# Kernel optimization log

Hardware: AMD Instinct MI355X
Metric: run time of the kernel (lower is better)

The kernel has to match this reference:

```python
import jax, jax.numpy as jnp
import numpy as np

B = 512      # batch
T = 16       # tokens per instruction
V = 1000     # vocab
E = 4        # num_experts
K = 1        # active experts per layer
NLAYERS = 3
TOPK_LOGIC = 32


def _conv(x, w, b, stride=2):
    # x: [B,Cin,H,W], w: [Cout,Cin,3,3] (OIHW), padding=1, stride=2
    y = jax.lax.conv_general_dilated(
        x, w, window_strides=(stride, stride), padding=((1, 1), (1, 1)),
        dimension_numbers=('NCHW', 'OIHW', 'NCHW'))
    return y + b[None, :, None, None]


def _gated_conv(x, w, b, gate):
    # w: [E,Cout,Cin,3,3], b: [E,Cout], gate: [B,E] 0/1 mask
    # Faithful to original: all experts computed densely, then masked.
    outs = jax.vmap(lambda wi, bi: _conv(x, wi, bi))(w, b)  # [E,B,Cout,H',W']
    return jnp.einsum('ebchw,be->bchw', outs, gate)


def _topk_mask(logits, k):
    # 0/1 mask with ones at the top-k positions along the last axis
    _, idx = jax.lax.top_k(logits, k)
    return jnp.sum(jax.nn.one_hot(idx, logits.shape[-1], dtype=logits.dtype), axis=-2)


def setup_inputs() -> dict:
    key = jax.random.key(0)
    ks = jax.random.split(key, 16)
    def rn(k, shape, s=0.05):
        return jax.random.normal(k, shape, jnp.float32) * s
    return dict(
        img=jax.random.normal(ks[0], (B, 12, 56, 56), jnp.float32),
        text=jax.random.randint(ks[1], (B, T), 0, V),
        prev_action=jax.random.randint(ks[2], (B,), 0, 7),
        emb_table=rn(ks[3], (V, 32), 1.0),
        r_w1=rn(ks[4], (32, 64)), r_b1=jnp.zeros((64,), jnp.float32),
        r_w2=rn(ks[5], (64, NLAYERS * E)), r_b2=jnp.zeros((NLAYERS * E,), jnp.float32),
        l_w1=rn(ks[6], (32, 64)), l_b1=jnp.zeros((64,), jnp.float32),
        l_w2=rn(ks[7], (64, 256)), l_b2=jnp.zeros((256,), jnp.float32),
        c1_w=rn(ks[8], (E, 32, 12, 3, 3)), c1_b=jnp.zeros((E, 32), jnp.float32),
        c2_w=rn(ks[9], (E, 64, 32, 3, 3)), c2_b=jnp.zeros((E, 64), jnp.float32),
        c3_w=rn(ks[10], (E, 128, 64, 3, 3)), c3_b=jnp.zeros((E, 128), jnp.float32),
        act_emb=rn(ks[11], (7, 16), 1.0),
        f_w=rn(ks[12], (6272 + 32 + 16, 256)), f_b=jnp.zeros((256,), jnp.float32),
        h_w=rn(ks[13], (256, 5)), h_b=jnp.zeros((5,), jnp.float32),
    )


def reference(img, text, prev_action, emb_table, r_w1, r_b1, r_w2, r_b2,
              l_w1, l_b1, l_w2, l_b2, c1_w, c1_b, c2_w, c2_b, c3_w, c3_b,
              act_emb, f_w, f_b, h_w, h_b):
    # EmbeddingBag(mode='mean') over token dim
    lang = jnp.mean(emb_table[text], axis=1)                      # [B,32]
    # Router: MLP -> [B,3,E] logits, top-k scatter -> 0/1 mask
    rlog = (jax.nn.relu(lang @ r_w1 + r_b1) @ r_w2 + r_b2).reshape(-1, NLAYERS, E)
    masks = _topk_mask(rlog, K)                                   # [B,3,E]
    x = jax.nn.relu(_gated_conv(img, c1_w, c1_b, masks[:, 0, :])) # [B,32,28,28]
    x = jax.nn.relu(_gated_conv(x, c2_w, c2_b, masks[:, 1, :]))   # [B,64,14,14]
    x = jax.nn.relu(_gated_conv(x, c3_w, c3_b, masks[:, 2, :]))   # [B,128,7,7]
    vis = x.reshape(x.shape[0], -1)                               # [B,6272]
    act = act_emb[prev_action]                                    # [B,16]
    fused = jnp.concatenate([vis, lang, act], axis=1)             # [B,6320]
    hidden = fused @ f_w + f_b                                    # [B,256]
    logic = jax.nn.relu(lang @ l_w1 + l_b1) @ l_w2 + l_b2         # [B,256]
    lmask = _topk_mask(logic, TOPK_LOGIC)                         # [B,256]
    out = jax.nn.relu(hidden * lmask)                             # dropout is identity in eval
    logits = out @ h_w + h_b                                      # [B,5]
    return logits, rlog
```

## Files before the change

### kernel.cpp

```cpp
#include <hip/hip_runtime.h>
#include <hip/hip_bf16.h>


typedef __bf16 bf16x8 __attribute__((ext_vector_type(8)));
typedef float f32x4 __attribute__((ext_vector_type(4)));

__device__ __forceinline__ unsigned short f2bf(float f) {
  union { float f; unsigned u; } v; v.f = f;
  unsigned r = v.u + 0x7FFFu + ((v.u >> 16) & 1u);
  return (unsigned short)(r >> 16);
}

__device__ __forceinline__ int wswz(int b) { return b ^ (((b >> 7) & 3) << 4); }

__global__ __launch_bounds__(256) void prep_kernel(
    const int* __restrict__ text, const float* __restrict__ emb,
    const float* __restrict__ r_w1, const float* __restrict__ r_b1,
    const float* __restrict__ r_w2, const float* __restrict__ r_b2,
    const float* __restrict__ l_w1, const float* __restrict__ l_b1,
    const float* __restrict__ l_w2, const float* __restrict__ l_b2,
    const float* __restrict__ act_emb, const int* __restrict__ pa,
    const float* __restrict__ c1_w, const float* __restrict__ c2_w,
    const float* __restrict__ c3_w, const float* __restrict__ fw,
    float* __restrict__ rlog_out, int* __restrict__ eidx, float* __restrict__ lmask,
    unsigned short* __restrict__ tailb,
    unsigned short* __restrict__ wb1, unsigned short* __restrict__ wb2,
    unsigned short* __restrict__ wb3, unsigned short* __restrict__ fwT) {
  __shared__ __align__(16) char shm[64 * 72 * 2];
  const int blk = blockIdx.x;
  const int tid = threadIdx.x;

  if (blk < 512) {
    int b = blk;
    int t = tid;
    __shared__ float lg[32];
    __shared__ float hr[64];
    __shared__ float hl[64];
    __shared__ float rl[12];
    __shared__ float lgc[256];

    if (t < 32) {
      const int* tb = text + b * 16;
      float s = 0.f;
#pragma unroll
      for (int tok = 0; tok < 16; ++tok) s += emb[tb[tok] * 32 + t];
      lg[t] = s * 0.0625f;
    }
    __syncthreads();

    if (t < 64) {
      float s1 = r_b1[t], s2 = l_b1[t];
      for (int k = 0; k < 32; ++k) {
        float lv = lg[k];
        s1 += lv * r_w1[k * 64 + t];
        s2 += lv * l_w1[k * 64 + t];
      }
      hr[t] = fmaxf(s1, 0.f);
      hl[t] = fmaxf(s2, 0.f);
    }
    if (t < 64) {
      float v = 0.f;
      if (t < 32) v = lg[t];
      else if (t < 48) v = act_emb[pa[b] * 16 + (t - 32)];
      tailb[b * 64 + t] = f2bf(v);
    }
    __syncthreads();

    if (t < 12) {
      float s = r_b2[t];
      for (int k = 0; k < 64; ++k) s += hr[k] * r_w2[k * 12 + t];
      rl[t] = s;
      rlog_out[b * 12 + t] = s;
    }
    {
      float s = l_b2[t];
      for (int k = 0; k < 64; ++k) s += hl[k] * l_w2[k * 256 + t];
      lgc[t] = s;
    }
    __syncthreads();

    if (t < 3) {
      int best = 0;
      float bv = rl[t * 4];
      for (int e = 1; e < 4; ++e) {
        float v = rl[t * 4 + e];
        if (v > bv) { bv = v; best = e; }
      }
      eidx[b * 3 + t] = best;
    }
    {
      float v = lgc[t];
      int cnt = 0;
      for (int k = 0; k < 256; ++k) {
        float u = lgc[k];
        cnt += (u > v) || (u == v && k < t);
      }
      lmask[b * 256 + t] = (cnt < 32) ? 1.f : 0.f;
    }
  } else if (blk < 2080) {
    int idx = (blk - 512) * 256 + tid;
    if (idx < 24576) {
      int k = idx % 192, ec = idx / 192;
      float v = 0.f;
      if (k < 144) {
        int g = k >> 4, ci = k & 15;
        if (ci < 12) v = c1_w[ec * 108 + ci * 9 + g];
      }
      wb1[idx] = f2bf(v);
    } else if (idx < 106496) {
      int i2 = idx - 24576;
      int k = i2 % 320, ec = i2 / 320;
      float v = 0.f;
      if (k < 288) {
        int g = k >> 5, ci = k & 31;
        v = c2_w[ec * 288 + ci * 9 + g];
      }
      wb2[i2] = f2bf(v);
    } else {
      int i3 = idx - 106496;
      int k = i3 % 576, ec = i3 / 576;
      int g = k >> 6, ci = k & 63;
      wb3[i3] = f2bf(c3_w[ec * 576 + ci * 9 + g]);
    }
  } else {
    unsigned short(*tl)[72] = (unsigned short(*)[72])shm;
    int fb = blk - 2080;
    int kblk = fb >> 2, nblk = fb & 3;
    int n0 = nblk * 64;
    int k0 = kblk * 64;
    int rl = tid >> 2;
    int c4 = (tid & 3) * 16;
    int srow;
    bool valid;
    if (kblk < 98) {
      int p = kblk >> 1;
      int c0 = (kblk & 1) * 64;
      srow = (c0 + rl) * 49 + p;
      valid = true;
    } else {
      srow = 6272 + rl;
      valid = (rl < 48);
    }
#pragma unroll
    for (int h = 0; h < 4; ++h) {
      float4 v = valid ? *(const float4*)&fw[(size_t)srow * 256 + n0 + c4 + h * 4]
                       : (float4){0.f, 0.f, 0.f, 0.f};
      tl[rl][c4 + h * 4 + 0] = f2bf(v.x);
      tl[rl][c4 + h * 4 + 1] = f2bf(v.y);
      tl[rl][c4 + h * 4 + 2] = f2bf(v.z);
      tl[rl][c4 + h * 4 + 3] = f2bf(v.w);
    }
    __syncthreads();
    int nloc = tid >> 2;
    int kc = (tid & 3) * 16;
    unsigned short vv[16];
#pragma unroll
    for (int i = 0; i < 16; ++i) vv[i] = tl[kc + i][nloc];
    unsigned short* dst = fwT + (size_t)(n0 + nloc) * 6336 + k0 + kc;
    *(uint4*)dst = *(const uint4*)&vv[0];
    *(uint4*)(dst + 8) = *(const uint4*)&vv[8];
  }
}

__global__ __launch_bounds__(256) void bucket_kernel(const int* __restrict__ eidx,
                                                     int* __restrict__ cnt,
                                                     int* __restrict__ perm) {
  int l = blockIdx.x;
  __shared__ int el[512];
  __shared__ int cc[4];
  int t = threadIdx.x;
  el[t] = eidx[t * 3 + l];
  el[t + 256] = eidx[(t + 256) * 3 + l];
  __syncthreads();
  if (t < 4) {
    int c = 0;
    for (int b = 0; b < 512; ++b) c += (el[b] == t);
    cc[t] = c;
    cnt[l * 4 + t] = c;
  }
  __syncthreads();
#pragma unroll
  for (int rep = 0; rep < 2; ++rep) {
    int b = t + rep * 256;
    int e = el[b];
    int rank = 0;
    for (int bp = 0; bp < b; ++bp) rank += (el[bp] == e);
    int off = 0;
    for (int ee = 0; ee < e; ++ee) off += cc[ee];
    perm[l * 512 + off + rank] = b;
  }
}

__global__ __launch_bounds__(256) void conv1_fused(
    const float* __restrict__ img, const unsigned short* __restrict__ wb,
    const float* __restrict__ bias, const int* __restrict__ eidx,
    unsigned short* __restrict__ out) {
  const int s = blockIdx.x / 7;
  const int t = blockIdx.x % 7;
  const int e = eidx[s * 3];
  __shared__ __align__(16) char win[25536];
  __shared__ __align__(16) char ldsB[3 * 4096];
  const int tid = threadIdx.x;
  const int lane = tid & 63;
  const int wid = tid >> 6;
  const int wm0 = wid * 32;

  const int p0 = t * 128;
  const int ohmin = p0 / 28;
  const int ih0 = ohmin * 2 - 1;

  {
    uint4 z; z.x = z.y = z.z = z.w = 0u;
    for (int i = tid; i < 1596; i += 256) ((uint4*)win)[i] = z;
  }
  {
    const unsigned short* wbe = wb + e * (32 * 192);
#pragma unroll
    for (int c = 0; c < 3; ++c) {
      int cc = tid + 256 * c;
      int n = cc / 24, cb = cc - n * 24;
      int kt = cb >> 3, cbl = cb & 7;
      uint4 v = *(const uint4*)(wbe + n * 192 + cb * 8);
      *(uint4*)(ldsB + kt * 4096 + n * 128 + ((cbl * 16) ^ ((n & 7) << 4))) = v;
    }
  }
  __syncthreads();

  for (int task = tid; task < 312; task += 256) {
    int row = task >> 1, half = task & 1;
    int ci = row / 13, ihl = row - ci * 13;
    int ih = ih0 + ihl;
    if ((unsigned)ih < 56u) {
      const float* src = img + (size_t)s * 37632 + ci * 3136 + ih * 56 + half * 28;
      int base = (ihl * 57 + half * 28 + 1) * 32 + ci * 2;
#pragma unroll
      for (int u = 0; u < 7; ++u) {
        float4 v = *(const float4*)(src + u * 4);
        unsigned short w4[4] = {f2bf(v.x), f2bf(v.y), f2bf(v.z), f2bf(v.w)};
#pragma unroll
        for (int q = 0; q < 4; ++q) {
          int bp = base + (u * 4 + q) * 32;
          *(unsigned short*)(win + wswz(bp)) = w4[q];
        }
      }
    }
  }

  int ohl[2], owr[2];
#pragma unroll
  for (int mf = 0; mf < 2; ++mf) {
    int m = wm0 + mf * 16 + (lane & 15);
    int p = p0 + m;
    if (p > 783) p = 783;
    int oh = p / 28;
    owr[mf] = p - oh * 28;
    ohl[mf] = (oh - ohmin) * 2;
  }
  const int lg = lane >> 4;
  const int ci0 = (lg & 1) * 8;
  const int lgh = lg >> 1;
  int brdo[2], brx[2];
#pragma unroll
  for (int nf = 0; nf < 2; ++nf) {
    int n = nf * 16 + (lane & 15);
    brdo[nf] = n * 128;
    brx[nf] = (n & 7) << 4;
  }

  f32x4 acc[2][2];
#pragma unroll
  for (int mf = 0; mf < 2; ++mf)
#pragma unroll
    for (int nf = 0; nf < 2; ++nf) acc[mf][nf] = (f32x4){0.f, 0.f, 0.f, 0.f};

  __syncthreads();

#pragma unroll
  for (int kt = 0; kt < 3; ++kt) {
#pragma unroll
    for (int ks = 0; ks < 2; ++ks) {
      const int g = kt * 4 + ks * 2 + lgh;
      const int kh = g / 3;
      const int kw = g - kh * 3;
      const bool gv = (g < 9);
      bf16x8 af[2];
#pragma unroll
      for (int mf = 0; mf < 2; ++mf) {
        int iwp = owr[mf] * 2 + kw;
        int ihl = ohl[mf] + kh;
        int bp = gv ? ((ihl * 57 + iwp) * 32 + ci0 * 2)
                    : (13 * 57 * 32 + ci0 * 2);
        af[mf] = __builtin_bit_cast(bf16x8, *(const uint4*)(win + wswz(bp)));
      }
      bf16x8 bfv[2];
      const int cb = ks * 64 + ((lane >> 4) << 4);
#pragma unroll
      for (int nf = 0; nf < 2; ++nf)
        bfv[nf] = __builtin_bit_cast(bf16x8,
            *(const uint4*)(ldsB + kt * 4096 + brdo[nf] + (cb ^ brx[nf])));
#pragma unroll
      for (int mf = 0; mf < 2; ++mf)
#pragma unroll
        for (int nf = 0; nf < 2; ++nf)
          acc[mf][nf] = __builtin_amdgcn_mfma_f32_16x16x32_bf16(af[mf], bfv[nf], acc[mf][nf], 0, 0, 0);
    }
  }

  const int col = lane & 15;
  const int rg = (lane >> 4) * 4;
  const float b0 = bias[e * 32 + col];
  const float b1 = bias[e * 32 + 16 + col];
#pragma unroll
  for (int mf = 0; mf < 2; ++mf)
#pragma unroll
    for (int r = 0; r < 4; ++r) {
      int m = wm0 + mf * 16 + rg + r;
      int p = p0 + m;
      if (p < 784) {
        size_t ob = ((size_t)s * 784 + p) * 32;
        out[ob + col]      = f2bf(fmaxf(acc[mf][0][r] + b0, 0.f));
        out[ob + 16 + col] = f2bf(fmaxf(acc[mf][1][r] + b1, 0.f));
      }
    }
}

template<int CIN, int H, int OH, int KREAL, int KP, int COUT,
         int WGM, int WGN, int MF, int NF>
__global__ __launch_bounds__(256) void conv_mfma(
    const unsigned short* __restrict__ in, const unsigned short* __restrict__ wb,
    const float* __restrict__ bias, const int* __restrict__ cnt,
    const int* __restrict__ perm, unsigned short* __restrict__ out) {
  constexpr int PerS = OH * OH;
  constexpr int BM = WGM * MF * 16;
  constexpr int BN = WGN * NF * 16;
  constexpr int AJ = BM / 32;
  constexpr int KT = KP / 64;
  constexpr int W = H;
  constexpr int BCH = BN / 32;

  int bm = blockIdx.x;
  int e = 0, row0 = 0, rows = 0;
  bool found = false;
  {
    int acc = 0, ebase = 0;
#pragma unroll
    for (int ee = 0; ee < 4; ++ee) {
      int er = cnt[ee] * PerS;
      int te = (er + BM - 1) / BM;
      if (!found && bm < acc + te) {
        e = ee;
        row0 = ebase + (bm - acc) * BM;
        rows = er - (bm - acc) * BM;
        if (rows > BM) rows = BM;
        found = true;
      }
      acc += te;
      ebase += er;
    }
  }
  if (!found) return;

  __shared__ __align__(16) char lds[BM * 128 + BN * 128];
  char* ldsB = lds + BM * 128;
  const int tid = threadIdx.x;
  const int lane = tid & 63;
  const int wid = tid >> 6;
  const int wm0 = (wid / WGN) * (MF * 16);
  const int wn0 = (wid % WGN) * (NF * 16);
  const int c16 = tid & 7;

  int ihc[AJ], iwc[AJ], abase[AJ], adso[AJ];
#pragma unroll
  for (int j = 0; j < AJ; ++j) {
    int r = (tid >> 3) + 32 * j;
    int gr = row0 + r;
    const int MAXR = 512 * PerS - 1;
    if (gr > MAXR) gr = MAXR;
    int sord = gr / PerS;
    int p = gr - sord * PerS;
    int s = perm[sord];
    int oh = p / OH, ow = p - oh * OH;
    ihc[j] = oh * 2 - 1;
    iwc[j] = ow * 2 - 1;
    abase[j] = s * (H * W);
    adso[j] = r * 128 + ((c16 * 16) ^ ((r & 7) << 4));
  }
  const unsigned short* wbe = wb + (size_t)e * COUT * KP;
  int bgo[BCH], bdso[BCH];
#pragma unroll
  for (int c = 0; c < BCH; ++c) {
    int cc = tid + 256 * c;
    int n = cc >> 3, cb = cc & 7;
    bgo[c] = n * KP + cb * 8;
    bdso[c] = n * 128 + ((cb * 16) ^ ((n & 7) << 4));
  }
  int ardo[MF], arx[MF], brdo[NF], brx[NF];
#pragma unroll
  for (int mf = 0; mf < MF; ++mf) {
    int r = wm0 + mf * 16 + (lane & 15);
    ardo[mf] = r * 128;
    arx[mf] = (r & 7) << 4;
  }
#pragma unroll
  for (int nf = 0; nf < NF; ++nf) {
    int n = wn0 + nf * 16 + (lane & 15);
    brdo[nf] = n * 128;
    brx[nf] = (n & 7) << 4;
  }

  auto loadA = [&](int kt, int j) -> uint4 {
    uint4 z; z.x = z.y = z.z = z.w = 0u;
    int kbase = kt * 64 + c16 * 8;
    if (kbase >= KREAL) return z;
    int g = kbase / CIN;
    int ci0 = kbase - g * CIN;
    int kh = g / 3, kw = g - (g / 3) * 3;
    int ih = ihc[j] + kh, iw = iwc[j] + kw;
    if ((unsigned)ih >= (unsigned)H || (unsigned)iw >= (unsigned)W) return z;
    const unsigned short* p = in + ((size_t)(abase[j] + ih * W + iw) * CIN + ci0);
    return *(const uint4*)p;
  };

  uint4 rA[AJ], rB[BCH];
#pragma unroll
  for (int j = 0; j < AJ; ++j) rA[j] = loadA(0, j);
#pragma unroll
  for (int c = 0; c < BCH; ++c) rB[c] = *(const uint4*)(wbe + bgo[c]);

  f32x4 acc[MF][NF];
#pragma unroll
  for (int mf = 0; mf < MF; ++mf)
#pragma unroll
    for (int nf = 0; nf < NF; ++nf) acc[mf][nf] = (f32x4){0.f, 0.f, 0.f, 0.f};

  for (int kt = 0; kt < KT; ++kt) {
    __syncthreads();
#pragma unroll
    for (int j = 0; j < AJ; ++j) *(uint4*)(lds + adso[j]) = rA[j];
#pragma unroll
    for (int c = 0; c < BCH; ++c) *(uint4*)(ldsB + bdso[c]) = rB[c];
    __syncthreads();
    if (kt + 1 < KT) {
#pragma unroll
      for (int j = 0; j < AJ; ++j) rA[j] = loadA(kt + 1, j);
#pragma unroll
      for (int c = 0; c < BCH; ++c) rB[c] = *(const uint4*)(wbe + bgo[c] + (kt + 1) * 64);
    }
#pragma unroll
    for (int ks = 0; ks < 2; ++ks) {
      int cb = ks * 64 + ((lane >> 4) << 4);
      bf16x8 af[MF], bfv[NF];
#pragma unroll
      for (int mf = 0; mf < MF; ++mf)
        af[mf] = __builtin_bit_cast(bf16x8, *(const uint4*)(lds + ardo[mf] + (cb ^ arx[mf])));
#pragma unroll
      for (int nf = 0; nf < NF; ++nf)
        bfv[nf] = __builtin_bit_cast(bf16x8, *(const uint4*)(ldsB + brdo[nf] + (cb ^ brx[nf])));
#pragma unroll
      for (int mf = 0; mf < MF; ++mf)
#pragma unroll
        for (int nf = 0; nf < NF; ++nf)
          acc[mf][nf] = __builtin_amdgcn_mfma_f32_16x16x32_bf16(af[mf], bfv[nf], acc[mf][nf], 0, 0, 0);
    }
  }

  const int col = lane & 15;
  const int rg = (lane >> 4) * 4;
#pragma unroll
  for (int mf = 0; mf < MF; ++mf) {
#pragma unroll
    for (int r = 0; r < 4; ++r) {
      int m = wm0 + mf * 16 + rg + r;
      if (m < rows) {
        int gr = row0 + m;
        int sord = gr / PerS;
        int p = gr - sord * PerS;
        int s = perm[sord];
        size_t ob = ((size_t)s * PerS + p) * COUT;
#pragma unroll
        for (int nf = 0; nf < NF; ++nf) {
          int co = wn0 + nf * 16 + col;
          float v = acc[mf][nf][r] + bias[e * COUT + co];
          out[ob + co] = f2bf(fmaxf(v, 0.f));
        }
      }
    }
  }
}

__global__ __launch_bounds__(256) void fgemm_kernel(
    const unsigned short* __restrict__ x3, const unsigned short* __restrict__ tail,
    const unsigned short* __restrict__ fwT, float* __restrict__ partial) {
  constexpr int MF = 2, NF = 2;
  const int row0 = blockIdx.x * 64;
  const int nc0 = blockIdx.y * 64;
  const int kz = blockIdx.z * 704;
  __shared__ __align__(16) char lds[64 * 128 + 64 * 128];
  char* ldsB = lds + 64 * 128;
  const int tid = threadIdx.x;
  const int lane = tid & 63;
  const int wid = tid >> 6;
  const int wm0 = (wid >> 1) * 32;
  const int wn0 = (wid & 1) * 32;
  const int c16 = tid & 7;
  int arow[2], adso[2];
#pragma unroll
  for (int j = 0; j < 2; ++j) {
    int r = (tid >> 3) + 32 * j;
    arow[j] = row0 + r;
    adso[j] = r * 128 + ((c16 * 16) ^ ((r & 7) << 4));
  }
  int bgo[2], bdso[2];
#pragma unroll
  for (int c = 0; c < 2; ++c) {
    int cc = tid + 256 * c;
    int n = cc >> 3, cb = cc & 7;
    bgo[c] = (nc0 + n) * 6336 + kz + cb * 8;
    bdso[c] = n * 128 + ((cb * 16) ^ ((n & 7) << 4));
  }
  int ardo[MF], arx[MF], brdo[NF], brx[NF];
#pragma unroll
  for (int mf = 0; mf < MF; ++mf) {
    int r = wm0 + mf * 16 + (lane & 15);
    ardo[mf] = r * 128; arx[mf] = (r & 7) << 4;
  }
#pragma unroll
  for (int nf = 0; nf < NF; ++nf) {
    int n = wn0 + nf * 16 + (lane & 15);
    brdo[nf] = n * 128; brx[nf] = (n & 7) << 4;
  }
  auto loadA = [&](int kt, int j) -> uint4 {
    int k = kz + kt * 64 + c16 * 8;
    const unsigned short* p;
    if (k < 6272) p = x3 + (size_t)arow[j] * 6272 + k;
    else p = tail + arow[j] * 64 + (k - 6272);
    return *(const uint4*)p;
  };
  uint4 rA[2], rB[2];
#pragma unroll
  for (int j = 0; j < 2; ++j) rA[j] = loadA(0, j);
#pragma unroll
  for (int c = 0; c < 2; ++c) rB[c] = *(const uint4*)(fwT + bgo[c]);
  f32x4 acc[MF][NF];
#pragma unroll
  for (int mf = 0; mf < MF; ++mf)
#pragma unroll
    for (int nf = 0; nf < NF; ++nf) acc[mf][nf] = (f32x4){0.f, 0.f, 0.f, 0.f};

  for (int kt = 0; kt < 11; ++kt) {
    __syncthreads();
#pragma unroll
    for (int j = 0; j < 2; ++j) *(uint4*)(lds + adso[j]) = rA[j];
#pragma unroll
    for (int c = 0; c < 2; ++c) *(uint4*)(ldsB + bdso[c]) = rB[c];
    __syncthreads();
    if (kt + 1 < 11) {
#pragma unroll
      for (int j = 0; j < 2; ++j) rA[j] = loadA(kt + 1, j);
#pragma unroll
      for (int c = 0; c < 2; ++c) rB[c] = *(const uint4*)(fwT + bgo[c] + (kt + 1) * 64);
    }
#pragma unroll
    for (int ks = 0; ks < 2; ++ks) {
      int cb = ks * 64 + ((lane >> 4) << 4);
      bf16x8 af[MF], bfv[NF];
#pragma unroll
      for (int mf = 0; mf < MF; ++mf)
        af[mf] = __builtin_bit_cast(bf16x8, *(const uint4*)(lds + ardo[mf] + (cb ^ arx[mf])));
#pragma unroll
      for (int nf = 0; nf < NF; ++nf)
        bfv[nf] = __builtin_bit_cast(bf16x8, *(const uint4*)(ldsB + brdo[nf] + (cb ^ brx[nf])));
#pragma unroll
      for (int mf = 0; mf < MF; ++mf)
#pragma unroll
        for (int nf = 0; nf < NF; ++nf)
          acc[mf][nf] = __builtin_amdgcn_mfma_f32_16x16x32_bf16(af[mf], bfv[nf], acc[mf][nf], 0, 0, 0);
    }
  }
  const int col = lane & 15;
  const int rg = (lane >> 4) * 4;
  float* pz = partial + (size_t)blockIdx.z * 131072;
#pragma unroll
  for (int mf = 0; mf < MF; ++mf)
#pragma unroll
    for (int r = 0; r < 4; ++r) {
      int m = wm0 + mf * 16 + rg + r;
      int grow = row0 + m;
#pragma unroll
      for (int nf = 0; nf < NF; ++nf) {
        int n = nc0 + wn0 + nf * 16 + col;
        pz[grow * 256 + n] = acc[mf][nf][r];
      }
    }
}

__global__ __launch_bounds__(256) void reduce_head(const float* __restrict__ part,
                                                   const float* __restrict__ f_b,
                                                   const float* __restrict__ lmask,
                                                   const float* __restrict__ h_w,
                                                   const float* __restrict__ h_b,
                                                   float* __restrict__ logits) {
  int b = blockIdx.x, t = threadIdx.x;
  float s = f_b[t];
#pragma unroll
  for (int z = 0; z < 9; ++z) s += part[z * 131072 + b * 256 + t];
  __shared__ float o[256];
  o[t] = (lmask[b * 256 + t] != 0.f) ? fmaxf(s, 0.f) : 0.f;
  __syncthreads();
  if (t < 5) {
    float v = h_b[t];
    for (int n = 0; n < 256; ++n) v += o[n] * h_w[n * 5 + t];
    logits[b * 5 + t] = v;
  }
}

extern "C" void kernel_launch(void* const* d_in, const int* in_sizes, int n_in,
                              void* d_out, int out_size, void* d_ws, size_t ws_size,
                              hipStream_t stream) {
  (void)in_sizes; (void)n_in; (void)out_size; (void)ws_size;
  const float* img       = (const float*)d_in[0];
  const int*   text      = (const int*)d_in[1];
  const int*   pa        = (const int*)d_in[2];
  const float* emb_table = (const float*)d_in[3];
  const float* r_w1 = (const float*)d_in[4];
  const float* r_b1 = (const float*)d_in[5];
  const float* r_w2 = (const float*)d_in[6];
  const float* r_b2 = (const float*)d_in[7];
  const float* l_w1 = (const float*)d_in[8];
  const float* l_b1 = (const float*)d_in[9];
  const float* l_w2 = (const float*)d_in[10];
  const float* l_b2 = (const float*)d_in[11];
  const float* c1_w = (const float*)d_in[12];
  const float* c1_b = (const float*)d_in[13];
  const float* c2_w = (const float*)d_in[14];
  const float* c2_b = (const float*)d_in[15];
  const float* c3_w = (const float*)d_in[16];
  const float* c3_b = (const float*)d_in[17];
  const float* act_emb = (const float*)d_in[18];
  const float* f_w = (const float*)d_in[19];
  const float* f_b = (const float*)d_in[20];
  const float* h_w = (const float*)d_in[21];
  const float* h_b = (const float*)d_in[22];

  float* outf   = (float*)d_out;
  float* logits = outf;
  float* rlog   = outf + 2560;

  char* cur = (char*)d_ws;
  auto alloc = [&](size_t bytes) { char* r = cur; cur += (bytes + 255) & ~(size_t)255; return r; };
  float* lmask   = (float*)alloc(131072 * 4);
  int* eidx      = (int*)alloc(1536 * 4);
  int* cnt       = (int*)alloc(12 * 4);
  int* perm      = (int*)alloc(1536 * 4);
  unsigned short* wb1  = (unsigned short*)alloc((size_t)24576 * 2);
  unsigned short* wb2  = (unsigned short*)alloc((size_t)81920 * 2);
  unsigned short* wb3  = (unsigned short*)alloc((size_t)294912 * 2);
  unsigned short* fwT  = (unsigned short*)alloc((size_t)1622016 * 2);
  unsigned short* tailb= (unsigned short*)alloc((size_t)32768 * 2);
  unsigned short* x1b  = (unsigned short*)alloc((size_t)12845056 * 2);
  unsigned short* x2b  = (unsigned short*)alloc((size_t)6422528 * 2);
  unsigned short* x3b  = (unsigned short*)alloc((size_t)3211264 * 2);
  float* partial       = (float*)alloc((size_t)9 * 131072 * 4);

  prep_kernel<<<2476, 256, 0, stream>>>(text, emb_table,
                                        r_w1, r_b1, r_w2, r_b2,
                                        l_w1, l_b1, l_w2, l_b2,
                                        act_emb, pa,
                                        c1_w, c2_w, c3_w, f_w,
                                        rlog, eidx, lmask, tailb,
                                        wb1, wb2, wb3, fwT);
  bucket_kernel<<<3, 256, 0, stream>>>(eidx, cnt, perm);

  conv1_fused<<<3584, 256, 0, stream>>>(img, wb1, c1_b, eidx, x1b);
  conv_mfma<32, 28, 14, 288, 320, 64, 2, 2, 4, 2>
      <<<787, 256, 0, stream>>>(x1b, wb2, c2_b, cnt + 4, perm + 512, x2b);
  conv_mfma<64, 14, 7, 576, 576, 128, 1, 4, 4, 2>
      <<<395, 256, 0, stream>>>(x2b, wb3, c3_b, cnt + 8, perm + 1024, x3b);

  fgemm_kernel<<<dim3(8, 4, 9), 256, 0, stream>>>(x3b, tailb, fwT, partial);
  reduce_head<<<512, 256, 0, stream>>>(partial, f_b, lmask, h_w, h_b, logits);
}
```

Measured before the change: 148.0 us.

## Fold bucketing into conv1, widen fwT transpose blocks, rework conv1 image load

Removes the separate bucket_kernel launch by running the expert bucketing in three extra blocks appended to the conv1 grid. The f_w transpose now handles a full 64x256 tile per block, so far fewer blocks are launched and a larger LDS tile is used. Conv1's image staging is changed so each thread gathers four channels for one pixel and writes 8 bytes into LDS at once. The fgemm store loop is hardcoded to NF=2, which is only correct if NF equals 2.

```diff
diff --git a/kernel.cpp b/kernel.cpp
--- a/kernel.cpp
+++ b/kernel.cpp
@@ -26,7 +26,7 @@
     unsigned short* __restrict__ tailb,
     unsigned short* __restrict__ wb1, unsigned short* __restrict__ wb2,
     unsigned short* __restrict__ wb3, unsigned short* __restrict__ fwT) {
-  __shared__ __align__(16) char shm[64 * 72 * 2];
+  __shared__ __align__(16) unsigned short tl2[64][272];
   const int blk = blockIdx.x;
   const int tid = threadIdx.x;
 
@@ -123,84 +123,85 @@
       wb3[i3] = f2bf(c3_w[ec * 576 + ci * 9 + g]);
     }
   } else {
-    unsigned short(*tl)[72] = (unsigned short(*)[72])shm;
-    int fb = blk - 2080;
-    int kblk = fb >> 2, nblk = fb & 3;
-    int n0 = nblk * 64;
-    int k0 = kblk * 64;
-    int rl = tid >> 2;
-    int c4 = (tid & 3) * 16;
-    int srow;
-    bool valid;
-    if (kblk < 98) {
-      int p = kblk >> 1;
-      int c0 = (kblk & 1) * 64;
-      srow = (c0 + rl) * 49 + p;
-      valid = true;
-    } else {
-      srow = 6272 + rl;
-      valid = (rl < 48);
-    }
-#pragma unroll
-    for (int h = 0; h < 4; ++h) {
-      float4 v = valid ? *(const float4*)&fw[(size_t)srow * 256 + n0 + c4 + h * 4]
-                       : (float4){0.f, 0.f, 0.f, 0.f};
-      tl[rl][c4 + h * 4 + 0] = f2bf(v.x);
-      tl[rl][c4 + h * 4 + 1] = f2bf(v.y);
-      tl[rl][c4 + h * 4 + 2] = f2bf(v.z);
-      tl[rl][c4 + h * 4 + 3] = f2bf(v.w);
-    }
-    __syncthreads();
-    int nloc = tid >> 2;
-    int kc = (tid & 3) * 16;
-    unsigned short vv[16];
-#pragma unroll
-    for (int i = 0; i < 16; ++i) vv[i] = tl[kc + i][nloc];
-    unsigned short* dst = fwT + (size_t)(n0 + nloc) * 6336 + k0 + kc;
-    *(uint4*)dst = *(const uint4*)&vv[0];
-    *(uint4*)(dst + 8) = *(const uint4*)&vv[8];
-  }
-}
-
-__global__ __launch_bounds__(256) void bucket_kernel(const int* __restrict__ eidx,
-                                                     int* __restrict__ cnt,
-                                                     int* __restrict__ perm) {
-  int l = blockIdx.x;
-  __shared__ int el[512];
-  __shared__ int cc[4];
-  int t = threadIdx.x;
-  el[t] = eidx[t * 3 + l];
-  el[t + 256] = eidx[(t + 256) * 3 + l];
-  __syncthreads();
-  if (t < 4) {
-    int c = 0;
-    for (int b = 0; b < 512; ++b) c += (el[b] == t);
-    cc[t] = c;
-    cnt[l * 4 + t] = c;
-  }
-  __syncthreads();
-#pragma unroll
-  for (int rep = 0; rep < 2; ++rep) {
-    int b = t + rep * 256;
-    int e = el[b];
-    int rank = 0;
-    for (int bp = 0; bp < b; ++bp) rank += (el[bp] == e);
-    int off = 0;
-    for (int ee = 0; ee < e; ++ee) off += cc[ee];
-    perm[l * 512 + off + rank] = b;
+    int kb = blk - 2080;
+    int k0 = kb * 64;
+#pragma unroll
+    for (int rg = 0; rg < 4; ++rg) {
+      int rl = rg * 16 + (tid >> 4);
+      int srow;
+      bool valid;
+      if (kb < 98) {
+        srow = ((kb & 1) * 64 + rl) * 49 + (kb >> 1);
+        valid = true;
+      } else {
+        srow = 6272 + rl;
+        valid = (rl < 48);
+      }
+#pragma unroll
+      for (int c = 0; c < 4; ++c) {
+        int col = ((tid & 15) + c * 16) * 4;
+        float4 v = valid ? *(const float4*)&fw[(size_t)srow * 256 + col]
+                         : (float4){0.f, 0.f, 0.f, 0.f};
+        tl2[rl][col + 0] = f2bf(v.x);
+        tl2[rl][col + 1] = f2bf(v.y);
+        tl2[rl][col + 2] = f2bf(v.z);
+        tl2[rl][col + 3] = f2bf(v.w);
+      }
+    }
+    __syncthreads();
+#pragma unroll
+    for (int np = 0; np < 4; ++np) {
+      int n = np * 64 + (tid >> 2);
+      int kc = (tid & 3) * 16;
+      unsigned short vv[16];
+#pragma unroll
+      for (int i = 0; i < 16; ++i) vv[i] = tl2[kc + i][n];
+      unsigned short* dst = fwT + (size_t)n * 6336 + k0 + kc;
+      *(uint4*)dst = *(const uint4*)&vv[0];
+      *(uint4*)(dst + 8) = *(const uint4*)&vv[8];
+    }
   }
 }
 
 __global__ __launch_bounds__(256) void conv1_fused(
     const float* __restrict__ img, const unsigned short* __restrict__ wb,
     const float* __restrict__ bias, const int* __restrict__ eidx,
-    unsigned short* __restrict__ out) {
+    unsigned short* __restrict__ out, int* __restrict__ cnt,
+    int* __restrict__ perm) {
+  __shared__ __align__(16) char win[25536];
+  __shared__ __align__(16) char ldsB[3 * 4096];
+  const int tid = threadIdx.x;
+
+  if (blockIdx.x >= 3584) {
+    int* el = (int*)win;
+    int* cc = el + 512;
+    int l = blockIdx.x - 3584;
+    el[tid] = eidx[tid * 3 + l];
+    el[tid + 256] = eidx[(tid + 256) * 3 + l];
+    __syncthreads();
+    if (tid < 4) {
+      int c = 0;
+      for (int b = 0; b < 512; ++b) c += (el[b] == tid);
+      cc[tid] = c;
+      cnt[l * 4 + tid] = c;
+    }
+    __syncthreads();
+#pragma unroll
+    for (int rep = 0; rep < 2; ++rep) {
+      int b = tid + rep * 256;
+      int e = el[b];
+      int rank = 0;
+      for (int bp = 0; bp < b; ++bp) rank += (el[bp] == e);
+      int off = 0;
+      for (int ee = 0; ee < e; ++ee) off += cc[ee];
+      perm[l * 512 + off + rank] = b;
+    }
+    return;
+  }
+
   const int s = blockIdx.x / 7;
   const int t = blockIdx.x % 7;
   const int e = eidx[s * 3];
-  __shared__ __align__(16) char win[25536];
-  __shared__ __align__(16) char ldsB[3 * 4096];
-  const int tid = threadIdx.x;
   const int lane = tid & 63;
   const int wid = tid >> 6;
   const int wm0 = wid * 32;
@@ -226,23 +227,19 @@
   }
   __syncthreads();
 
-  for (int task = tid; task < 312; task += 256) {
-    int row = task >> 1, half = task & 1;
-    int ci = row / 13, ihl = row - ci * 13;
+  const float* ibase = img + (size_t)s * 37632;
+  for (int c = tid; c < 2184; c += 256) {
+    int q = c / 728;
+    int rem = c - q * 728;
+    int ihl = rem / 56;
+    int iw = rem - ihl * 56;
     int ih = ih0 + ihl;
     if ((unsigned)ih < 56u) {
-      const float* src = img + (size_t)s * 37632 + ci * 3136 + ih * 56 + half * 28;
-      int base = (ihl * 57 + half * 28 + 1) * 32 + ci * 2;
-#pragma unroll
-      for (int u = 0; u < 7; ++u) {
-        float4 v = *(const float4*)(src + u * 4);
-        unsigned short w4[4] = {f2bf(v.x), f2bf(v.y), f2bf(v.z), f2bf(v.w)};
-#pragma unroll
-        for (int q = 0; q < 4; ++q) {
-          int bp = base + (u * 4 + q) * 32;
-          *(unsigned short*)(win + wswz(bp)) = w4[q];
-        }
-      }
+      const float* src = ibase + q * 4 * 3136 + ih * 56 + iw;
+      unsigned short w4[4] = {f2bf(src[0]), f2bf(src[3136]),
+                              f2bf(src[6272]), f2bf(src[9408])};
+      int bp = (ihl * 57 + iw + 1) * 32 + q * 8;
+      *(unsigned long long*)(win + wswz(bp)) = *(const unsigned long long*)w4;
     }
   }
 
@@ -587,7 +584,7 @@
       int m = wm0 + mf * 16 + rg + r;
       int grow = row0 + m;
 #pragma unroll
-      for (int nf = 0; nf < NF; ++nf) {
+      for (int nf = 0; nf < 2; ++nf) {
         int n = nc0 + wn0 + nf * 16 + col;
         pz[grow * 256 + n] = acc[mf][nf][r];
       }
@@ -662,16 +659,15 @@
   unsigned short* x3b  = (unsigned short*)alloc((size_t)3211264 * 2);
   float* partial       = (float*)alloc((size_t)9 * 131072 * 4);
 
-  prep_kernel<<<2476, 256, 0, stream>>>(text, emb_table,
+  prep_kernel<<<2179, 256, 0, stream>>>(text, emb_table,
                                         r_w1, r_b1, r_w2, r_b2,
                                         l_w1, l_b1, l_w2, l_b2,
                                         act_emb, pa,
                                         c1_w, c2_w, c3_w, f_w,
                                         rlog, eidx, lmask, tailb,
                                         wb1, wb2, wb3, fwT);
-  bucket_kernel<<<3, 256, 0, stream>>>(eidx, cnt, perm);
-
-  conv1_fused<<<3584, 256, 0, stream>>>(img, wb1, c1_b, eidx, x1b);
+
+  conv1_fused<<<3587, 256, 0, stream>>>(img, wb1, c1_b, eidx, x1b, cnt, perm);
   conv_mfma<32, 28, 14, 288, 320, 64, 2, 2, 4, 2>
       <<<787, 256, 0, stream>>>(x1b, wb2, c2_b, cnt + 4, perm + 512, x2b);
   conv_mfma<64, 14, 7, 576, 576, 128, 1, 4, 4, 2>
```

Result: faster. 144.7 us (-2.2%).
